# Performance work log

Hardware: AMD Instinct MI355X
Metric: run time of the kernel (lower is better)

## Reference

```python
import jax, jax.numpy as jnp
import numpy as np

B, S, DM, H, SD = 8, 2048, 512, 8, 64
INNER = H * SD
HID = 4 * DM
EPS = 1e-5


def setup_inputs() -> dict:
    key = jax.random.key(0)
    ks = jax.random.split(key, 12)
    p = lambda k, sh: jax.random.normal(k, sh, dtype=jnp.float32) * 0.02
    return {
        "x": jax.random.normal(ks[0], (B, S, DM), dtype=jnp.float32),
        "norm_g": jnp.ones((DM,), jnp.float32),
        "norm_b": jnp.zeros((DM,), jnp.float32),
        "ffn_norm_g": jnp.ones((DM,), jnp.float32),
        "ffn_norm_b": jnp.zeros((DM,), jnp.float32),
        "Wa": p(ks[1], (INNER, DM)),
        "Wb": p(ks[2], (INNER, DM)),
        "Wql": p(ks[3], (INNER, DM)),
        "Wqr": p(ks[4], (INNER, DM)),
        "Wsd": p(ks[5], (H, DM)),
        "bsd": jnp.zeros((H,), jnp.float32),
        "Wpd": p(ks[6], (H, DM)),
        "bpd": jnp.zeros((H,), jnp.float32),
        "Wout": p(ks[7], (DM, INNER)),
        "W1": p(ks[8], (HID, DM)),
        "b1": jnp.zeros((HID,), jnp.float32),
        "W2": p(ks[9], (DM, HID)),
        "b2": jnp.zeros((DM,), jnp.float32),
    }


def _ln(x, g, b):
    m = x.mean(-1, keepdims=True)
    v = ((x - m) ** 2).mean(-1, keepdims=True)
    return (x - m) / jnp.sqrt(v + EPS) * g + b


def reference(x, norm_g, norm_b, ffn_norm_g, ffn_norm_b, Wa, Wb, Wql, Wqr,
              Wsd, bsd, Wpd, bpd, Wout, W1, b1, W2, b2):
    n = _ln(x, norm_g, norm_b)  # [B,S,DM]
    # project, reshape to heads, move time axis first for scan: [S,B,H,SD]
    tm = lambda t: t.reshape(B, S, H, SD).transpose(1, 0, 2, 3)
    a_all = tm(jnp.tanh(n @ Wa.T))
    b_all = tm(jnp.tanh(n @ Wb.T))
    ql_all = tm(jnp.tanh(n @ Wql.T))
    qr_all = tm(jnp.tanh(n @ Wqr.T))
    sd_all = jax.nn.sigmoid(n @ Wsd.T + bsd).transpose(1, 0, 2)[..., None]        # [S,B,H,1]
    pd_all = jax.nn.sigmoid(n @ Wpd.T + bpd).transpose(1, 0, 2)[..., None, None]  # [S,B,H,1,1]

    def step(carry, inp):
        state, pair = carry  # state [B,H,SD], pair [B,H,SD,SD]
        at, bt, qlt, sdt, pdt = inp
        prev = state
        state = sdt * state + (1.0 - sdt) * at
        pair = pdt * pair + (1.0 - pdt) * jnp.einsum('bhd,bhe->bhde', prev, bt)
        lc = jnp.einsum('bhde,bhd->bhe', pair, qlt)  # left context [B,H,SD]
        return (state, pair), lc

    init = (jnp.zeros((B, H, SD), x.dtype), jnp.zeros((B, H, SD, SD), x.dtype))
    _, lc = jax.lax.scan(step, init, (a_all, b_all, ql_all, sd_all, pd_all))  # [S,B,H,SD]

    mixed = ((lc * qr_all).transpose(1, 0, 2, 3).reshape(B, S, INNER)) @ Wout.T  # [B,S,DM]
    r = x + mixed  # dropout is identity in eval
    h = jax.nn.gelu(_ln(r, ffn_norm_g, ffn_norm_b) @ W1.T + b1, approximate=False)
    return r + h @ W2.T + b2
```

## Files before the change

kernel.cpp:

```cpp
#include <hip/hip_runtime.h>
#include <cstdint>
#include <cstddef>

#define B_    8
#define S_    2048
#define DM_   512
#define H_    8
#define SD_   64
#define HID_  2048
#define ROWS  (B_*S_)
#define BH    (B_*H_)
#define NCHUNK 32
#define CLEN   64
#define EPS_  1e-5f

typedef __bf16 bf16x8 __attribute__((ext_vector_type(8)));
typedef float  floatx4 __attribute__((ext_vector_type(4)));

static __device__ __forceinline__ float bf2f(unsigned short h){
  union { unsigned int u; float f; } v; v.u = ((unsigned int)h) << 16; return v.f;
}
static __device__ __forceinline__ unsigned short f2bf(float f){
  union { float f; unsigned int u; } v; v.f = f;
  unsigned int r = v.u + 0x7fffu + ((v.u >> 16) & 1u);
  return (unsigned short)(r >> 16);
}
static __device__ __forceinline__ float fast_tanh(float x){
  float ax = fabsf(x);
  float e  = __expf(2.f*ax);
  float t  = 1.f - 2.f/(e+1.f);
  return copysignf(t, x);
}
static __device__ __forceinline__ float sigmoidf_(float z){
  return 1.f/(1.f + expf(-z));
}
static __device__ __forceinline__ float gelu_exact(float x){
  return 0.5f*x*(1.f + erff(x*0.70710678118654752440f));
}
static __device__ __forceinline__ void gld_lds16(const unsigned short* g, unsigned short* lds){
  __builtin_amdgcn_global_load_lds(
      (const __attribute__((address_space(1))) void*)g,
      (__attribute__((address_space(3))) void*)lds,
      16, 0, 0);
}
static __device__ __forceinline__ int swz(int row, int col){
  return row*64 + (((col>>3) ^ (row&7))<<3) + (col&7);
}

__global__ __launch_bounds__(256) void cvt_weights(
    const float* __restrict__ wa, const float* __restrict__ wb,
    const float* __restrict__ wql, const float* __restrict__ wqr,
    const float* __restrict__ wout, const float* __restrict__ w1,
    const float* __restrict__ w2,
    unsigned short* __restrict__ wcat, unsigned short* __restrict__ woutb,
    unsigned short* __restrict__ w1b, unsigned short* __restrict__ w2b){
  int i = blockIdx.x*256 + threadIdx.x;
  const float* s; unsigned short* d; int base;
  if      (i <  65536){ s=wa;   d=wcat;          base=i; }
  else if (i < 131072){ s=wb;   d=wcat+262144;   base=i-65536; }
  else if (i < 196608){ s=wql;  d=wcat+524288;   base=i-131072; }
  else if (i < 262144){ s=wqr;  d=wcat+786432;   base=i-196608; }
  else if (i < 327680){ s=wout; d=woutb;         base=i-262144; }
  else if (i < 589824){ s=w1;   d=w1b;           base=i-327680; }
  else                { s=w2;   d=w2b;           base=i-589824; }
  float4 v = ((const float4*)s)[base];
  ushort4 o; o.x=f2bf(v.x); o.y=f2bf(v.y); o.z=f2bf(v.z); o.w=f2bf(v.w);
  ((ushort4*)d)[base] = o;
}

__global__ __launch_bounds__(64) void ln_gates(
    const float* __restrict__ x, const float* __restrict__ gam, const float* __restrict__ bet,
    const float* __restrict__ Wsd, const float* __restrict__ bsd,
    const float* __restrict__ Wpd, const float* __restrict__ bpd,
    unsigned short* __restrict__ nbf, float* __restrict__ sdo, float* __restrict__ pdo){
  const int row = blockIdx.x, l = threadIdx.x;
  const float* xr = x + (size_t)row*DM_;
  float4 v0 = ((const float4*)xr)[l*2];
  float4 v1 = ((const float4*)xr)[l*2+1];
  float v[8] = {v0.x,v0.y,v0.z,v0.w,v1.x,v1.y,v1.z,v1.w};
  float s = 0.f;
  #pragma unroll
  for (int i=0;i<8;++i) s += v[i];
  #pragma unroll
  for (int m=1;m<64;m<<=1) s += __shfl_xor(s, m);
  const float mean = s * (1.f/512.f);
  float q = 0.f;
  #pragma unroll
  for (int i=0;i<8;++i){ float d = v[i]-mean; q += d*d; }
  #pragma unroll
  for (int m=1;m<64;m<<=1) q += __shfl_xor(q, m);
  const float rstd = rsqrtf(q*(1.f/512.f) + EPS_);
  float4 g0 = ((const float4*)gam)[l*2], g1 = ((const float4*)gam)[l*2+1];
  float4 b0 = ((const float4*)bet)[l*2], b1 = ((const float4*)bet)[l*2+1];
  float gg[8] = {g0.x,g0.y,g0.z,g0.w,g1.x,g1.y,g1.z,g1.w};
  float bb[8] = {b0.x,b0.y,b0.z,b0.w,b1.x,b1.y,b1.z,b1.w};
  float n[8];
  #pragma unroll
  for (int i=0;i<8;++i) n[i] = (v[i]-mean)*rstd*gg[i] + bb[i];
  ushort4 o0, o1;
  o0.x=f2bf(n[0]); o0.y=f2bf(n[1]); o0.z=f2bf(n[2]); o0.w=f2bf(n[3]);
  o1.x=f2bf(n[4]); o1.y=f2bf(n[5]); o1.z=f2bf(n[6]); o1.w=f2bf(n[7]);
  ((ushort4*)(nbf + (size_t)row*DM_))[l*2]   = o0;
  ((ushort4*)(nbf + (size_t)row*DM_))[l*2+1] = o1;
  float acc[16];
  #pragma unroll
  for (int hh=0; hh<8; ++hh){
    const float4* ws = (const float4*)(Wsd + hh*DM_) + l*2;
    const float4* wp = (const float4*)(Wpd + hh*DM_) + l*2;
    float4 a0=ws[0], a1=ws[1], p0=wp[0], p1=wp[1];
    acc[hh]   = n[0]*a0.x+n[1]*a0.y+n[2]*a0.z+n[3]*a0.w+n[4]*a1.x+n[5]*a1.y+n[6]*a1.z+n[7]*a1.w;
    acc[8+hh] = n[0]*p0.x+n[1]*p0.y+n[2]*p0.z+n[3]*p0.w+n[4]*p1.x+n[5]*p1.y+n[6]*p1.z+n[7]*p1.w;
  }
  #pragma unroll
  for (int k=0;k<16;++k){
    float a = acc[k];
    #pragma unroll
    for (int m=1;m<64;m<<=1) a += __shfl_xor(a, m);
    acc[k] = a;
  }
  if (l==0){
    #pragma unroll
    for (int hh=0; hh<8; ++hh){
      sdo[row*8+hh] = sigmoidf_(acc[hh]   + bsd[hh]);
      pdo[row*8+hh] = sigmoidf_(acc[8+hh] + bpd[hh]);
    }
  }
}

__global__ __launch_bounds__(64) void ln_plain(
    const float* __restrict__ x, const float* __restrict__ gam, const float* __restrict__ bet,
    unsigned short* __restrict__ ob){
  const int row = blockIdx.x, l = threadIdx.x;
  const float* xr = x + (size_t)row*DM_;
  float4 v0 = ((const float4*)xr)[l*2];
  float4 v1 = ((const float4*)xr)[l*2+1];
  float v[8] = {v0.x,v0.y,v0.z,v0.w,v1.x,v1.y,v1.z,v1.w};
  float s = 0.f;
  #pragma unroll
  for (int i=0;i<8;++i) s += v[i];
  #pragma unroll
  for (int m=1;m<64;m<<=1) s += __shfl_xor(s, m);
  const float mean = s * (1.f/512.f);
  float q = 0.f;
  #pragma unroll
  for (int i=0;i<8;++i){ float d = v[i]-mean; q += d*d; }
  #pragma unroll
  for (int m=1;m<64;m<<=1) q += __shfl_xor(q, m);
  const float rstd = rsqrtf(q*(1.f/512.f) + EPS_);
  float4 g0 = ((const float4*)gam)[l*2], g1 = ((const float4*)gam)[l*2+1];
  float4 b0 = ((const float4*)bet)[l*2], b1 = ((const float4*)bet)[l*2+1];
  float gg[8] = {g0.x,g0.y,g0.z,g0.w,g1.x,g1.y,g1.z,g1.w};
  float bb[8] = {b0.x,b0.y,b0.z,b0.w,b1.x,b1.y,b1.z,b1.w};
  ushort4 o0, o1;
  float n0=(v[0]-mean)*rstd*gg[0]+bb[0], n1=(v[1]-mean)*rstd*gg[1]+bb[1];
  float n2=(v[2]-mean)*rstd*gg[2]+bb[2], n3=(v[3]-mean)*rstd*gg[3]+bb[3];
  float n4=(v[4]-mean)*rstd*gg[4]+bb[4], n5=(v[5]-mean)*rstd*gg[5]+bb[5];
  float n6=(v[6]-mean)*rstd*gg[6]+bb[6], n7=(v[7]-mean)*rstd*gg[7]+bb[7];
  o0.x=f2bf(n0); o0.y=f2bf(n1); o0.z=f2bf(n2); o0.w=f2bf(n3);
  o1.x=f2bf(n4); o1.y=f2bf(n5); o1.z=f2bf(n6); o1.w=f2bf(n7);
  ((ushort4*)(ob + (size_t)row*DM_))[l*2]   = o0;
  ((ushort4*)(ob + (size_t)row*DM_))[l*2+1] = o1;
}

template<int MODE>
__global__ __launch_bounds__(256) void gemm128(
    const unsigned short* __restrict__ A, const unsigned short* __restrict__ W,
    const float* __restrict__ bias, const float* __restrict__ resid,
    float* __restrict__ outf, unsigned short* __restrict__ outb,
    int N, int K){
  __shared__ __align__(16) unsigned short As[128*32];
  __shared__ __align__(16) unsigned short Ws[128*32];
  const int tid  = threadIdx.x;
  const int w    = tid >> 6;
  const int lane = tid & 63;
  const int mblk = blockIdx.x, nblk = blockIdx.y;
  const int lrow = lane >> 2;
  const int lcol = (lane & 3) * 8;
  const int mrow = (w >> 1) * 64;
  const int ncol = (w & 1) * 64;
  const int fr = lane & 15, fq = lane >> 4;

  floatx4 acc[4][4];
  #pragma unroll
  for (int i=0;i<4;++i)
    #pragma unroll
    for (int j=0;j<4;++j)
      acc[i][j] = (floatx4){0.f,0.f,0.f,0.f};

  for (int k0=0; k0<K; k0+=32){
    const unsigned short* ga0 = A + (size_t)(mblk*128 + w*32 + lrow)*K + k0 + lcol;
    const unsigned short* gw0 = W + (size_t)(nblk*128 + w*32 + lrow)*K + k0 + lcol;
    gld_lds16(ga0,                As + w*1024);
    gld_lds16(ga0 + (size_t)16*K, As + w*1024 + 512);
    gld_lds16(gw0,                Ws + w*1024);
    gld_lds16(gw0 + (size_t)16*K, Ws + w*1024 + 512);
    __syncthreads();
    bf16x8 af[4], bf[4];
    #pragma unroll
    for (int i=0;i<4;++i) af[i] = *(const bf16x8*)&As[(mrow + i*16 + fr)*32 + fq*8];
    #pragma unroll
    for (int j=0;j<4;++j) bf[j] = *(const bf16x8*)&Ws[(ncol + j*16 + fr)*32 + fq*8];
    #pragma unroll
    for (int i=0;i<4;++i)
      #pragma unroll
      for (int j=0;j<4;++j)
        acc[i][j] = __builtin_amdgcn_mfma_f32_16x16x32_bf16(af[i], bf[j], acc[i][j], 0, 0, 0);
    __syncthreads();
  }

  #pragma unroll
  for (int i=0;i<4;++i){
    const int grow_base = mblk*128 + mrow + i*16 + fq*4;
    #pragma unroll
    for (int j=0;j<4;++j){
      const int gcol = nblk*128 + ncol + j*16 + fr;
      float bias_v = 0.f;
      if (MODE==2 || MODE==3) bias_v = bias[gcol];
      #pragma unroll
      for (int r=0;r<4;++r){
        const size_t o = (size_t)(grow_base + r)*N + gcol;
        float v = acc[i][j][r];
        if      (MODE==0) outb[o] = f2bf(fast_tanh(v));
        else if (MODE==1) outf[o] = resid[o] + v;
        else if (MODE==2) outb[o] = f2bf(gelu_exact(v + bias_v));
        else              outf[o] = resid[o] + v + bias_v;
      }
    }
  }
}

__global__ __launch_bounds__(64) void state_local(
    const unsigned short* __restrict__ proj, const float* __restrict__ sdo,
    float* __restrict__ sloc, float* __restrict__ Sarr){
  const int c = blockIdx.x, bh = blockIdx.y, b = bh>>3, h = bh&7, d = threadIdx.x;
  float s = 0.f, S = 1.f;
  const int t0 = c*CLEN;
  #pragma unroll 4
  for (int j=0;j<CLEN;++j){
    const int t = t0 + j;
    float a  = bf2f(proj[((size_t)(b*S_+t))*2048 + h*64 + d]);
    float sv = sdo[(b*S_+t)*8 + h];
    s = sv*s + (1.f-sv)*a;
    S *= sv;
    sloc[((size_t)bh*S_ + t)*64 + d] = s;
    if (d==0) Sarr[bh*S_ + t] = S;
  }
}

__global__ __launch_bounds__(64) void state_combine(
    const float* __restrict__ sloc, const float* __restrict__ Sarr,
    float* __restrict__ sinit){
  const int bh = blockIdx.x, d = threadIdx.x;
  float acc = 0.f;
  for (int c=0;c<NCHUNK;++c){
    sinit[((size_t)c*BH + bh)*64 + d] = acc;
    const int te = c*CLEN + CLEN - 1;
    acc = Sarr[bh*S_ + te]*acc + sloc[((size_t)bh*S_ + te)*64 + d];
  }
}

__global__ __launch_bounds__(256) void prev_mat(
    const float* __restrict__ sloc, const float* __restrict__ Sarr,
    const float* __restrict__ sinit, unsigned short* __restrict__ prevb){
  const size_t idx = (size_t)blockIdx.x*256 + threadIdx.x;
  const int d  = (int)(idx & 63);
  const size_t bt = idx >> 6;
  const int t  = (int)(bt & (S_-1));
  const int bh = (int)(bt >> 11);
  const int c = t >> 6, j = t & 63;
  float init = sinit[((size_t)c*BH + bh)*64 + d];
  float p;
  if (j==0) p = init;
  else {
    const size_t pt = (size_t)bh*S_ + (t-1);
    p = Sarr[pt]*init + sloc[pt*64 + d];
  }
  prevb[idx] = f2bf(p);
}

__global__ __launch_bounds__(64) void pair_localm(
    const unsigned short* __restrict__ proj, const float* __restrict__ pdo,
    const unsigned short* __restrict__ prevb, float* __restrict__ pairbuf,
    float* __restrict__ Dprod){
  __shared__ __align__(16) unsigned short Bt[4096];
  __shared__ __align__(16) unsigned short Pt[4096];
  const int c=blockIdx.x, bh=blockIdx.y, b=bh>>3, h=bh&7, l=threadIdx.x;
  const int t = c*CLEN + l;
  float pd = pdo[(b*S_+t)*8 + h];
  float D = pd;
  #pragma unroll
  for (int m=1;m<64;m<<=1){ float o = __shfl_up(D, m); if (l>=m) D *= o; }
  const float Dend = __shfl(D, 63);
  const float cu = (Dend / D) * (1.f - pd);
  if (l==63) Dprod[c*BH+bh] = Dend;
  {
    const unsigned short* brow = proj  + ((size_t)(b*S_+t))*2048 + 512 + h*64;
    const unsigned short* prow = prevb + ((size_t)bh*S_ + t)*64;
    #pragma unroll
    for (int e8=0;e8<8;++e8){
      ushort4 u0 = *(const ushort4*)(brow + e8*8);
      ushort4 u1 = *(const ushort4*)(brow + e8*8 + 4);
      unsigned short vs[8] = {u0.x,u0.y,u0.z,u0.w,u1.x,u1.y,u1.z,u1.w};
      ushort4 p0 = *(const ushort4*)(prow + e8*8);
      ushort4 p1 = *(const ushort4*)(prow + e8*8 + 4);
      unsigned short ps[8] = {p0.x,p0.y,p0.z,p0.w,p1.x,p1.y,p1.z,p1.w};
      #pragma unroll
      for (int q=0;q<8;++q){
        const int r = e8*8+q;
        Bt[swz(r, l)] = f2bf(cu * bf2f(vs[q]));
        Pt[swz(r, l)] = ps[q];
      }
    }
  }
  __syncthreads();
  const int fr = l & 15, fq = l >> 4;
  floatx4 acc[4][4];
  #pragma unroll
  for (int i=0;i<4;++i)
    #pragma unroll
    for (int j=0;j<4;++j) acc[i][j] = (floatx4){0.f,0.f,0.f,0.f};
  #pragma unroll
  for (int kh=0;kh<2;++kh){
    bf16x8 af[4], bfr[4];
    #pragma unroll
    for (int i=0;i<4;++i) af[i]  = *(const bf16x8*)&Bt[swz(i*16+fr, kh*32+fq*8)];
    #pragma unroll
    for (int j=0;j<4;++j) bfr[j] = *(const bf16x8*)&Pt[swz(j*16+fr, kh*32+fq*8)];
    #pragma unroll
    for (int i=0;i<4;++i)
      #pragma unroll
      for (int j=0;j<4;++j)
        acc[i][j] = __builtin_amdgcn_mfma_f32_16x16x32_bf16(af[i], bfr[j], acc[i][j], 0, 0, 0);
  }
  float* outp = pairbuf + ((size_t)c*BH + bh)*4096;
  #pragma unroll
  for (int i=0;i<4;++i)
    #pragma unroll
    for (int j=0;j<4;++j)
      #pragma unroll
      for (int r=0;r<4;++r)
        outp[(i*16+fq*4+r)*64 + j*16+fr] = acc[i][j][r];
}

__global__ __launch_bounds__(256) void pair_combine(
    float* __restrict__ pairbuf, const float* __restrict__ Dprod){
  const int idx = blockIdx.x*256 + threadIdx.x;
  const int de = idx & 4095, bh = idx >> 12;
  float acc = 0.f;
  for (int c=0;c<NCHUNK;++c){
    const size_t o = ((size_t)c*BH + bh)*4096 + de;
    float loc = pairbuf[o];
    pairbuf[o] = acc;
    acc = Dprod[c*BH + bh]*acc + loc;
  }
}

__global__ __launch_bounds__(64) void pair_finalm(
    const unsigned short* __restrict__ proj, const float* __restrict__ pdo,
    const unsigned short* __restrict__ prevb, const float* __restrict__ pinit,
    unsigned short* __restrict__ lcqr){
  __shared__ __align__(16) unsigned short Bt[4096];
  __shared__ __align__(16) unsigned short Tb[4096];
  __shared__ __align__(16) float Dtl[64];
  __shared__ __align__(16) float cudl[64];
  const int c=blockIdx.x, bh=blockIdx.y, b=bh>>3, h=bh&7, l=threadIdx.x;
  const int t0 = c*CLEN;
  const int trow = t0 + l;
  float pd = pdo[(b*S_+trow)*8 + h];
  float D = pd;
  #pragma unroll
  for (int m=1;m<64;m<<=1){ float o = __shfl_up(D, m); if (l>=m) D *= o; }
  Dtl[l]  = D;
  cudl[l] = (1.f - pd) / D;
  {
    const unsigned short* brow = proj + ((size_t)(b*S_+trow))*2048 + 512 + h*64;
    #pragma unroll
    for (int e8=0;e8<8;++e8){
      ushort4 u0 = *(const ushort4*)(brow + e8*8);
      ushort4 u1 = *(const ushort4*)(brow + e8*8 + 4);
      unsigned short vs[8] = {u0.x,u0.y,u0.z,u0.w,u1.x,u1.y,u1.z,u1.w};
      #pragma unroll
      for (int q=0;q<8;++q) Bt[swz(e8*8+q, l)] = vs[q];
    }
  }
  __syncthreads();
  const int fr = l & 15, fq = l >> 4;
  bf16x8 qf[4][2], pf[4][2];
  #pragma unroll
  for (int i=0;i<4;++i)
    #pragma unroll
    for (int kh=0;kh<2;++kh){
      qf[i][kh] = *(const bf16x8*)(proj  + ((size_t)(b*S_ + t0 + i*16 + fr))*2048 + 1024 + h*64 + kh*32 + fq*8);
      pf[i][kh] = *(const bf16x8*)(prevb + ((size_t)(bh*S_ + t0 + i*16 + fr))*64  + kh*32 + fq*8);
    }
  floatx4 sacc[4][4];
  #pragma unroll
  for (int i=0;i<4;++i)
    #pragma unroll
    for (int j=0;j<4;++j) sacc[i][j] = (floatx4){0.f,0.f,0.f,0.f};
  #pragma unroll
  for (int kh=0;kh<2;++kh)
    #pragma unroll
    for (int i=0;i<4;++i)
      #pragma unroll
      for (int j=0;j<4;++j)
        sacc[i][j] = __builtin_amdgcn_mfma_f32_16x16x32_bf16(qf[i][kh], pf[j][kh], sacc[i][j], 0, 0, 0);
  float mycud[4];
  #pragma unroll
  for (int j=0;j<4;++j) mycud[j] = cudl[j*16+fr];
  #pragma unroll
  for (int i=0;i<4;++i){
    floatx4 dtv = *(const floatx4*)&Dtl[i*16+fq*4];
    #pragma unroll
    for (int j=0;j<4;++j){
      const int uu = j*16+fr;
      #pragma unroll
      for (int r=0;r<4;++r){
        const int tt = i*16+fq*4+r;
        float v = (uu<=tt) ? (sacc[i][j][r]*dtv[r])*mycud[j] : 0.f;
        Tb[swz(tt, uu)] = f2bf(v);
      }
    }
  }
  __syncthreads();
  floatx4 acc[4][4];
  #pragma unroll
  for (int i=0;i<4;++i)
    #pragma unroll
    for (int j=0;j<4;++j) acc[i][j] = (floatx4){0.f,0.f,0.f,0.f};
  #pragma unroll
  for (int kh=0;kh<2;++kh){
    bf16x8 af[4], bfr[4];
    #pragma unroll
    for (int i=0;i<4;++i) af[i]  = *(const bf16x8*)&Tb[swz(i*16+fr, kh*32+fq*8)];
    #pragma unroll
    for (int j=0;j<4;++j) bfr[j] = *(const bf16x8*)&Bt[swz(j*16+fr, kh*32+fq*8)];
    #pragma unroll
    for (int i=0;i<4;++i)
      #pragma unroll
      for (int j=0;j<4;++j)
        acc[i][j] = __builtin_amdgcn_mfma_f32_16x16x32_bf16(af[i], bfr[j], acc[i][j], 0, 0, 0);
  }
  {
    const float* ibase = pinit + ((size_t)c*BH + bh)*4096;
    #pragma unroll
    for (int kh=0;kh<2;++kh){
      bf16x8 qs[4], inf[4];
      #pragma unroll
      for (int i=0;i<4;++i){
        const float sc = Dtl[i*16+fr];
        #pragma unroll
        for (int e=0;e<8;++e) qs[i][e] = (__bf16)(sc * (float)qf[i][kh][e]);
      }
      #pragma unroll
      for (int j=0;j<4;++j){
        const float* ip = ibase + (j*16+fr)*64 + kh*32 + fq*8;
        float4 f0 = *(const float4*)ip;
        float4 f1 = *(const float4*)(ip+4);
        inf[j][0]=(__bf16)f0.x; inf[j][1]=(__bf16)f0.y; inf[j][2]=(__bf16)f0.z; inf[j][3]=(__bf16)f0.w;
        inf[j][4]=(__bf16)f1.x; inf[j][5]=(__bf16)f1.y; inf[j][6]=(__bf16)f1.z; inf[j][7]=(__bf16)f1.w;
      }
      #pragma unroll
      for (int i=0;i<4;++i)
        #pragma unroll
        for (int j=0;j<4;++j)
          acc[i][j] = __builtin_amdgcn_mfma_f32_16x16x32_bf16(qs[i], inf[j], acc[i][j], 0, 0, 0);
    }
  }
  __syncthreads();
  #pragma unroll
  for (int i=0;i<4;++i)
    #pragma unroll
    for (int j=0;j<4;++j)
      #pragma unroll
      for (int r=0;r<4;++r)
        Tb[swz(i*16+fq*4+r, j*16+fr)] = f2bf(acc[i][j][r]);
  __syncthreads();
  {
    const unsigned short* qrow = proj + ((size_t)(b*S_+trow))*2048 + 1536 + h*64;
    unsigned short* orow = lcqr + ((size_t)(b*S_+trow))*512 + h*64;
    #pragma unroll
    for (int e8=0;e8<8;++e8){
      bf16x8 lcv = *(const bf16x8*)&Tb[swz(l, e8*8)];
      ushort4 q0 = *(const ushort4*)(qrow + e8*8);
      ushort4 q1 = *(const ushort4*)(qrow + e8*8 + 4);
      unsigned short qv[8] = {q0.x,q0.y,q0.z,q0.w,q1.x,q1.y,q1.z,q1.w};
      ushort4 o0, o1;
      o0.x = f2bf((float)lcv[0]*bf2f(qv[0]));
      o0.y = f2bf((float)lcv[1]*bf2f(qv[1]));
      o0.z = f2bf((float)lcv[2]*bf2f(qv[2]));
      o0.w = f2bf((float)lcv[3]*bf2f(qv[3]));
      o1.x = f2bf((float)lcv[4]*bf2f(qv[4]));
      o1.y = f2bf((float)lcv[5]*bf2f(qv[5]));
      o1.z = f2bf((float)lcv[6]*bf2f(qv[6]));
      o1.w = f2bf((float)lcv[7]*bf2f(qv[7]));
      *(ushort4*)(orow + e8*8)     = o0;
      *(ushort4*)(orow + e8*8 + 4) = o1;
    }
  }
}

extern "C" void kernel_launch(void* const* d_in, const int* in_sizes, int n_in,
                              void* d_out, int out_size, void* d_ws, size_t ws_size,
                              hipStream_t stream){
  (void)in_sizes; (void)n_in; (void)out_size; (void)ws_size;
  const float* x    = (const float*)d_in[0];
  const float* ng   = (const float*)d_in[1];
  const float* nb   = (const float*)d_in[2];
  const float* fng  = (const float*)d_in[3];
  const float* fnb  = (const float*)d_in[4];
  const float* Wa   = (const float*)d_in[5];
  const float* Wb   = (const float*)d_in[6];
  const float* Wql  = (const float*)d_in[7];
  const float* Wqr  = (const float*)d_in[8];
  const float* Wsd  = (const float*)d_in[9];
  const float* bsd  = (const float*)d_in[10];
  const float* Wpd  = (const float*)d_in[11];
  const float* bpd  = (const float*)d_in[12];
  const float* Wout = (const float*)d_in[13];
  const float* W1   = (const float*)d_in[14];
  const float* b1   = (const float*)d_in[15];
  const float* W2   = (const float*)d_in[16];
  const float* b2   = (const float*)d_in[17];
  float* out = (float*)d_out;
  char* ws = (char*)d_ws;

  size_t off = 0;
  auto alloc = [&](size_t bytes)->char*{ char* p = ws + off; off += (bytes + 255) & ~(size_t)255; return p; };
  char* RA = alloc((size_t)ROWS*DM_*2);
  char* RB = alloc((size_t)ROWS*2048*2);
  char* RD = alloc((size_t)BH*S_*64*4);
  char* RE = alloc((size_t)BH*S_*64*4);
  float* sdo   = (float*)alloc((size_t)ROWS*8*4);
  float* pdo   = (float*)alloc((size_t)ROWS*8*4);
  float* Sarr  = (float*)alloc((size_t)BH*S_*4);
  float* sinit = (float*)alloc((size_t)NCHUNK*BH*64*4);
  float* dprod = (float*)alloc((size_t)NCHUNK*BH*4);
  unsigned short* wcat  = (unsigned short*)alloc((size_t)2048*512*2);
  unsigned short* woutb = (unsigned short*)alloc((size_t)512*512*2);
  unsigned short* w1b   = (unsigned short*)alloc((size_t)2048*512*2);
  unsigned short* w2b   = (unsigned short*)alloc((size_t)512*2048*2);

  unsigned short* nbf   = (unsigned short*)RA;
  unsigned short* lcqr  = (unsigned short*)RA;
  unsigned short* nr    = (unsigned short*)RA;
  unsigned short* proj  = (unsigned short*)RB;
  unsigned short* hbuf  = (unsigned short*)RB;
  float* sloc  = (float*)RD;
  float* pairb = (float*)RD;
  unsigned short* prevb = (unsigned short*)RE;
  float* rbuf  = (float*)RE;

  cvt_weights<<<dim3(3328), dim3(256), 0, stream>>>(Wa,Wb,Wql,Wqr,Wout,W1,W2, wcat,woutb,w1b,w2b);
  ln_gates<<<dim3(ROWS), dim3(64), 0, stream>>>(x, ng, nb, Wsd, bsd, Wpd, bpd, nbf, sdo, pdo);
  gemm128<0><<<dim3(128,16), dim3(256), 0, stream>>>(nbf, wcat, nullptr, nullptr, nullptr, proj, 2048, 512);
  state_local<<<dim3(NCHUNK,BH), dim3(64), 0, stream>>>(proj, sdo, sloc, Sarr);
  state_combine<<<dim3(BH), dim3(64), 0, stream>>>(sloc, Sarr, sinit);
  prev_mat<<<dim3(32768), dim3(256), 0, stream>>>(sloc, Sarr, sinit, prevb);
  pair_localm<<<dim3(NCHUNK,BH), dim3(64), 0, stream>>>(proj, pdo, prevb, pairb, dprod);
  pair_combine<<<dim3(1024), dim3(256), 0, stream>>>(pairb, dprod);
  pair_finalm<<<dim3(NCHUNK,BH), dim3(64), 0, stream>>>(proj, pdo, prevb, pairb, lcqr);
  gemm128<1><<<dim3(128,4), dim3(256), 0, stream>>>(lcqr, woutb, nullptr, x, rbuf, nullptr, 512, 512);
  ln_plain<<<dim3(ROWS), dim3(64), 0, stream>>>(rbuf, fng, fnb, nr);
  gemm128<2><<<dim3(128,16), dim3(256), 0, stream>>>(nr, w1b, b1, nullptr, nullptr, hbuf, 2048, 512);
  gemm128<3><<<dim3(128,4), dim3(256), 0, stream>>>(hbuf, w2b, b2, rbuf, out, nullptr, 512, 2048);
}
```

Measured before the change: 471.7 us.

## Double GEMM K-tile with XOR-swizzled LDS and store local state in bf16

The GEMM main loop now loads a 64-wide K slice per iteration into an XOR-swizzled LDS layout, so there are half as many barriers per K and fewer LDS bank conflicts on fragment reads. The per-chunk local state scan writes its intermediate in bf16 instead of fp32 and emits chunk-end states into a separate fp32 buffer for the combine step. This halves that buffer's traffic at some precision cost in the prev computation. It also uses twice the LDS per GEMM block, which may lower occupancy.

Result: faster. 446.2 us (-5.4%).

```diff
diff --git a/kernel.cpp b/kernel.cpp
--- a/kernel.cpp
+++ b/kernel.cpp
@@ -168,18 +168,24 @@
     const float* __restrict__ bias, const float* __restrict__ resid,
     float* __restrict__ outf, unsigned short* __restrict__ outb,
     int N, int K){
-  __shared__ __align__(16) unsigned short As[128*32];
-  __shared__ __align__(16) unsigned short Ws[128*32];
+  __shared__ __align__(16) unsigned short As[128*64];
+  __shared__ __align__(16) unsigned short Ws[128*64];
   const int tid  = threadIdx.x;
   const int w    = tid >> 6;
   const int lane = tid & 63;
   const int mblk = blockIdx.x, nblk = blockIdx.y;
-  const int lrow = lane >> 2;
-  const int lcol = (lane & 3) * 8;
   const int mrow = (w >> 1) * 64;
   const int ncol = (w & 1) * 64;
   const int fr = lane & 15, fq = lane >> 4;
 
+  int srow[4], scol[4];
+  #pragma unroll
+  for (int q=0;q<4;++q){
+    const int p = q*256 + w*64 + lane;
+    srow[q] = p >> 3;
+    scol[q] = ((p & 7) ^ (srow[q] & 7)) * 8;
+  }
+
   floatx4 acc[4][4];
   #pragma unroll
   for (int i=0;i<4;++i)
@@ -187,24 +193,26 @@
     for (int j=0;j<4;++j)
       acc[i][j] = (floatx4){0.f,0.f,0.f,0.f};
 
-  for (int k0=0; k0<K; k0+=32){
-    const unsigned short* ga0 = A + (size_t)(mblk*128 + w*32 + lrow)*K + k0 + lcol;
-    const unsigned short* gw0 = W + (size_t)(nblk*128 + w*32 + lrow)*K + k0 + lcol;
-    gld_lds16(ga0,                As + w*1024);
-    gld_lds16(ga0 + (size_t)16*K, As + w*1024 + 512);
-    gld_lds16(gw0,                Ws + w*1024);
-    gld_lds16(gw0 + (size_t)16*K, Ws + w*1024 + 512);
+  for (int k0=0; k0<K; k0+=64){
+    #pragma unroll
+    for (int q=0;q<4;++q){
+      gld_lds16(A + (size_t)(mblk*128 + srow[q])*K + k0 + scol[q], As + (q*256 + w*64)*8);
+      gld_lds16(W + (size_t)(nblk*128 + srow[q])*K + k0 + scol[q], Ws + (q*256 + w*64)*8);
+    }
     __syncthreads();
-    bf16x8 af[4], bf[4];
-    #pragma unroll
-    for (int i=0;i<4;++i) af[i] = *(const bf16x8*)&As[(mrow + i*16 + fr)*32 + fq*8];
-    #pragma unroll
-    for (int j=0;j<4;++j) bf[j] = *(const bf16x8*)&Ws[(ncol + j*16 + fr)*32 + fq*8];
-    #pragma unroll
-    for (int i=0;i<4;++i)
-      #pragma unroll
-      for (int j=0;j<4;++j)
-        acc[i][j] = __builtin_amdgcn_mfma_f32_16x16x32_bf16(af[i], bf[j], acc[i][j], 0, 0, 0);
+    #pragma unroll
+    for (int kh=0;kh<2;++kh){
+      bf16x8 af[4], bf[4];
+      #pragma unroll
+      for (int i=0;i<4;++i) af[i] = *(const bf16x8*)&As[swz(mrow + i*16 + fr, kh*32 + fq*8)];
+      #pragma unroll
+      for (int j=0;j<4;++j) bf[j] = *(const bf16x8*)&Ws[swz(ncol + j*16 + fr, kh*32 + fq*8)];
+      #pragma unroll
+      for (int i=0;i<4;++i)
+        #pragma unroll
+        for (int j=0;j<4;++j)
+          acc[i][j] = __builtin_amdgcn_mfma_f32_16x16x32_bf16(af[i], bf[j], acc[i][j], 0, 0, 0);
+    }
     __syncthreads();
   }
 
@@ -231,7 +239,8 @@
 
 __global__ __launch_bounds__(64) void state_local(
     const unsigned short* __restrict__ proj, const float* __restrict__ sdo,
-    float* __restrict__ sloc, float* __restrict__ Sarr){
+    unsigned short* __restrict__ slocb, float* __restrict__ Sarr,
+    float* __restrict__ sEnd){
   const int c = blockIdx.x, bh = blockIdx.y, b = bh>>3, h = bh&7, d = threadIdx.x;
   float s = 0.f, S = 1.f;
   const int t0 = c*CLEN;
@@ -242,25 +251,26 @@
     float sv = sdo[(b*S_+t)*8 + h];
     s = sv*s + (1.f-sv)*a;
     S *= sv;
-    sloc[((size_t)bh*S_ + t)*64 + d] = s;
+    slocb[((size_t)bh*S_ + t)*64 + d] = f2bf(s);
     if (d==0) Sarr[bh*S_ + t] = S;
   }
+  sEnd[((size_t)c*BH + bh)*64 + d] = s;
 }
 
 __global__ __launch_bounds__(64) void state_combine(
-    const float* __restrict__ sloc, const float* __restrict__ Sarr,
+    const float* __restrict__ sEnd, const float* __restrict__ Sarr,
     float* __restrict__ sinit){
   const int bh = blockIdx.x, d = threadIdx.x;
   float acc = 0.f;
   for (int c=0;c<NCHUNK;++c){
     sinit[((size_t)c*BH + bh)*64 + d] = acc;
     const int te = c*CLEN + CLEN - 1;
-    acc = Sarr[bh*S_ + te]*acc + sloc[((size_t)bh*S_ + te)*64 + d];
+    acc = Sarr[bh*S_ + te]*acc + sEnd[((size_t)c*BH + bh)*64 + d];
   }
 }
 
 __global__ __launch_bounds__(256) void prev_mat(
-    const float* __restrict__ sloc, const float* __restrict__ Sarr,
+    const unsigned short* __restrict__ slocb, const float* __restrict__ Sarr,
     const float* __restrict__ sinit, unsigned short* __restrict__ prevb){
   const size_t idx = (size_t)blockIdx.x*256 + threadIdx.x;
   const int d  = (int)(idx & 63);
@@ -273,7 +283,7 @@
   if (j==0) p = init;
   else {
     const size_t pt = (size_t)bh*S_ + (t-1);
-    p = Sarr[pt]*init + sloc[pt*64 + d];
+    p = Sarr[pt]*init + bf2f(slocb[pt*64 + d]);
   }
   prevb[idx] = f2bf(p);
 }
@@ -535,6 +545,7 @@
   float* pdo   = (float*)alloc((size_t)ROWS*8*4);
   float* Sarr  = (float*)alloc((size_t)BH*S_*4);
   float* sinit = (float*)alloc((size_t)NCHUNK*BH*64*4);
+  float* sEnd  = (float*)alloc((size_t)NCHUNK*BH*64*4);
   float* dprod = (float*)alloc((size_t)NCHUNK*BH*4);
   unsigned short* wcat  = (unsigned short*)alloc((size_t)2048*512*2);
   unsigned short* woutb = (unsigned short*)alloc((size_t)512*512*2);
@@ -546,7 +557,7 @@
   unsigned short* nr    = (unsigned short*)RA;
   unsigned short* proj  = (unsigned short*)RB;
   unsigned short* hbuf  = (unsigned short*)RB;
-  float* sloc  = (float*)RD;
+  unsigned short* slocb = (unsigned short*)RD;
   float* pairb = (float*)RD;
   unsigned short* prevb = (unsigned short*)RE;
   float* rbuf  = (float*)RE;
@@ -554,9 +565,9 @@
   cvt_weights<<<dim3(3328), dim3(256), 0, stream>>>(Wa,Wb,Wql,Wqr,Wout,W1,W2, wcat,woutb,w1b,w2b);
   ln_gates<<<dim3(ROWS), dim3(64), 0, stream>>>(x, ng, nb, Wsd, bsd, Wpd, bpd, nbf, sdo, pdo);
   gemm128<0><<<dim3(128,16), dim3(256), 0, stream>>>(nbf, wcat, nullptr, nullptr, nullptr, proj, 2048, 512);
-  state_local<<<dim3(NCHUNK,BH), dim3(64), 0, stream>>>(proj, sdo, sloc, Sarr);
-  state_combine<<<dim3(BH), dim3(64), 0, stream>>>(sloc, Sarr, sinit);
-  prev_mat<<<dim3(32768), dim3(256), 0, stream>>>(sloc, Sarr, sinit, prevb);
+  state_local<<<dim3(NCHUNK,BH), dim3(64), 0, stream>>>(proj, sdo, slocb, Sarr, sEnd);
+  state_combine<<<dim3(BH), dim3(64), 0, stream>>>(sEnd, Sarr, sinit);
+  prev_mat<<<dim3(32768), dim3(256), 0, stream>>>(slocb, Sarr, sinit, prevb);
   pair_localm<<<dim3(NCHUNK,BH), dim3(64), 0, stream>>>(proj, pdo, prevb, pairb, dprod);
   pair_combine<<<dim3(1024), dim3(256), 0, stream>>>(pairb, dprod);
   pair_finalm<<<dim3(NCHUNK,BH), dim3(64), 0, stream>>>(proj, pdo, prevb, pairb, lcqr);
```
